# Optimization experiments

Hardware: AMD Instinct MI355X
Metric: run time of the kernel (lower is better)

Reference implementation:

```python
import jax, jax.numpy as jnp
import numpy as np

B, L, S, H, E, D = 2, 2048, 2048, 16, 64, 64


def setup_inputs() -> dict:
    key = jax.random.key(0)
    ks = jax.random.split(key, 6)
    return {
        "q1": jax.random.normal(ks[0], (B, L, H, E), dtype=jnp.float32),
        "k1": jax.random.normal(ks[1], (B, S, H, E), dtype=jnp.float32),
        "v1": jax.random.normal(ks[2], (B, S, H, D), dtype=jnp.float32),
        "q2": jax.random.normal(ks[3], (B, L, H, E), dtype=jnp.float32),
        "k2": jax.random.normal(ks[4], (B, S, H, E), dtype=jnp.float32),
        "v2": jax.random.normal(ks[5], (B, S, H, D), dtype=jnp.float32),
        "attn_mask": 0,  # accepted but unused by the original forward
    }


def reference(q1, k1, v1, q2, k2, v2, attn_mask):
    # scale = 1/sqrt(E) (self.scale is None in init_kwargs)
    scale = 1.0 / jnp.sqrt(jnp.asarray(q1.shape[-1], dtype=q1.dtype))
    # dual QK scores: [B,H,L,S]
    scores1 = jnp.einsum('blhe,bshe->bhls', q1, k1)
    scores2 = jnp.einsum('blhe,bshe->bhls', q2, k2)
    # eval-mode (dropout disabled for deterministic reference)
    A = jnp.tanh(scores1 * scale) * jax.nn.sigmoid(scores2 * scale)
    # weighted V matmul: [B,L,H,D]
    out = jnp.einsum('bhls,bshd->blhd', A, v1)
    return out
```

## Files before the change

kernel.cpp:

```cpp
#include <hip/hip_runtime.h>

constexpr int Bc = 2, Lc = 2048, Sc = 2048, Hc = 16, Ec = 64, Dc = 64;
constexpr int TILES = Sc / 64;
constexpr int NBH   = Bc * Hc;
constexpr size_t TILE_ELEMS = 4096;
constexpr size_t ARR_ELEMS  = (size_t)NBH * TILES * TILE_ELEMS;
constexpr size_t WS_NEED    = ARR_ELEMS * 2 * 3;

typedef float          f32x4  __attribute__((ext_vector_type(4)));
typedef __bf16         bf16x8 __attribute__((ext_vector_type(8)));
typedef unsigned short u16x8  __attribute__((ext_vector_type(8)));
typedef unsigned short u16x4  __attribute__((ext_vector_type(4)));
typedef unsigned int   u32x4  __attribute__((ext_vector_type(4)));
typedef unsigned int   u32x2  __attribute__((ext_vector_type(2)));

static __device__ __forceinline__ unsigned cvtpk(float lo, float hi) {
    unsigned r;
    asm("v_cvt_pk_bf16_f32 %0, %1, %2" : "=v"(r) : "v"(lo), "v"(hi));
    return r;
}

static __device__ __forceinline__ void gl2lds16(const void* g, void* l) {
    __builtin_amdgcn_global_load_lds(
        (const __attribute__((address_space(1))) unsigned int*)g,
        (__attribute__((address_space(3))) unsigned int*)l, 16, 0, 0);
}

static __device__ __forceinline__ float fexp2(float x) {
#if __has_builtin(__builtin_amdgcn_exp2f)
    return __builtin_amdgcn_exp2f(x);
#else
    return exp2f(x);
#endif
}

__global__ __launch_bounds__(256) void prepass_kernel(
    const float* __restrict__ k1, const float* __restrict__ k2,
    const float* __restrict__ v1,
    unsigned short* __restrict__ k1b, unsigned short* __restrict__ k2b,
    unsigned short* __restrict__ vb)
{
    __shared__ unsigned short vt[64 * 80];

    const int blk = blockIdx.x;
    const int st  = blk & 31;
    const int bh  = blk >> 5;
    const int b   = bh >> 4, h = bh & 15;
    const int s0  = st * 64;
    const size_t tileo = (size_t)blk * TILE_ELEMS;

    #pragma unroll
    for (int it = 0; it < 2; ++it) {
        int u  = threadIdx.x + it * 256;
        int s  = u >> 3, e8 = u & 7;
        size_t g = ((size_t)((b * Sc + s0 + s) * Hc + h)) * Ec + e8 * 8;

        float4 x0 = *reinterpret_cast<const float4*>(k1 + g);
        float4 x1 = *reinterpret_cast<const float4*>(k1 + g + 4);
        u32x4 o;
        o[0] = cvtpk(x0.x, x0.y); o[1] = cvtpk(x0.z, x0.w);
        o[2] = cvtpk(x1.x, x1.y); o[3] = cvtpk(x1.z, x1.w);
        *reinterpret_cast<u32x4*>(&k1b[tileo + (size_t)(s * 8 + (e8 ^ (s & 7))) * 8]) = o;

        x0 = *reinterpret_cast<const float4*>(k2 + g);
        x1 = *reinterpret_cast<const float4*>(k2 + g + 4);
        o[0] = cvtpk(x0.x, x0.y); o[1] = cvtpk(x0.z, x0.w);
        o[2] = cvtpk(x1.x, x1.y); o[3] = cvtpk(x1.z, x1.w);
        *reinterpret_cast<u32x4*>(&k2b[tileo + (size_t)(s * 8 + (e8 ^ (s & 7))) * 8]) = o;

        x0 = *reinterpret_cast<const float4*>(v1 + g);
        x1 = *reinterpret_cast<const float4*>(v1 + g + 4);
        o[0] = cvtpk(x0.x, x0.y); o[1] = cvtpk(x0.z, x0.w);
        o[2] = cvtpk(x1.x, x1.y); o[3] = cvtpk(x1.z, x1.w);
        *reinterpret_cast<u32x4*>(&vt[s * 80 + e8 * 8]) = o;
    }
    __syncthreads();

    #pragma unroll
    for (int it = 0; it < 2; ++it) {
        int u  = threadIdx.x + it * 256;
        int d  = u >> 3, sc8 = u & 7;
        u16x8 o;
        #pragma unroll
        for (int j = 0; j < 8; ++j) o[j] = vt[(sc8 * 8 + j) * 80 + d];
        *reinterpret_cast<u16x8*>(&vb[tileo + (size_t)(d * 8 + sc8) * 8]) = o;
    }
}

__global__ __launch_bounds__(256, 4) void fused_kernel(
    const float* __restrict__ q1, const float* __restrict__ q2,
    const unsigned short* __restrict__ k1b, const unsigned short* __restrict__ k2b,
    const unsigned short* __restrict__ vb, float* __restrict__ out)
{
    __shared__ unsigned short klds[2][2][4096];
    __shared__ unsigned int   pbounce[4][256];

    const int orig    = blockIdx.x;
    const int logical = (orig & 7) * 128 + (orig >> 3);
    const int lblk = logical & 31;
    const int bh   = logical >> 5;
    const int b    = bh >> 4, h = bh & 15;

    const int tid  = threadIdx.x;
    const int w    = tid >> 6;
    const int lane = tid & 63;
    const int lr   = lane & 15;
    const int lg   = lane >> 4;
    const int qsub = w >> 1;
    const int sh   = w & 1;

    constexpr float C1 = 0.36067376022224085f;
    constexpr float C2 = -0.18033688011112043f;
    bf16x8 a1[2][2], a2[2][2];
    #pragma unroll
    for (int qg = 0; qg < 2; ++qg) {
        const int    qrow  = lblk * 64 + qsub * 32 + qg * 16 + lr;
        const size_t qbase = ((size_t)((b * Lc + qrow) * Hc + h)) * Ec;
        #pragma unroll
        for (int es = 0; es < 2; ++es) {
            const float* p1 = q1 + qbase + es * 32 + lg * 8;
            const float* p2 = q2 + qbase + es * 32 + lg * 8;
            float4 x0 = *reinterpret_cast<const float4*>(p1);
            float4 x1 = *reinterpret_cast<const float4*>(p1 + 4);
            u32x4 o;
            o[0] = cvtpk(x0.x * C1, x0.y * C1); o[1] = cvtpk(x0.z * C1, x0.w * C1);
            o[2] = cvtpk(x1.x * C1, x1.y * C1); o[3] = cvtpk(x1.z * C1, x1.w * C1);
            a1[qg][es] = __builtin_bit_cast(bf16x8, o);
            x0 = *reinterpret_cast<const float4*>(p2);
            x1 = *reinterpret_cast<const float4*>(p2 + 4);
            o[0] = cvtpk(x0.x * C2, x0.y * C2); o[1] = cvtpk(x0.z * C2, x0.w * C2);
            o[2] = cvtpk(x1.x * C2, x1.y * C2); o[3] = cvtpk(x1.z * C2, x1.w * C2);
            a2[qg][es] = __builtin_bit_cast(bf16x8, o);
        }
    }

    f32x4 acc[2][4];
    #pragma unroll
    for (int qg = 0; qg < 2; ++qg)
        #pragma unroll
        for (int dt = 0; dt < 4; ++dt) acc[qg][dt] = (f32x4){0.f, 0.f, 0.f, 0.f};

    const unsigned short* k1g = k1b + (size_t)bh * TILES * TILE_ELEMS;
    const unsigned short* k2g = k2b + (size_t)bh * TILES * TILE_ELEMS;
    const unsigned short* vg  = vb  + (size_t)bh * TILES * TILE_ELEMS;
    unsigned int* pb = &pbounce[w][0];

    {
        const size_t tb = (size_t)tid * 8;
        gl2lds16(k1g + tb,        &klds[0][0][tid * 8]);
        gl2lds16(k1g + tb + 2048, &klds[0][0][tid * 8 + 2048]);
        gl2lds16(k2g + tb,        &klds[0][1][tid * 8]);
        gl2lds16(k2g + tb + 2048, &klds[0][1][tid * 8 + 2048]);
    }

    int cur = 0;
    for (int st = 0; st < TILES; ++st) {
        __syncthreads();
        if (st + 1 < TILES) {
            const size_t tb = (size_t)(st + 1) * TILE_ELEMS + tid * 8;
            const int nxt = cur ^ 1;
            gl2lds16(k1g + tb,        &klds[nxt][0][tid * 8]);
            gl2lds16(k1g + tb + 2048, &klds[nxt][0][tid * 8 + 2048]);
            gl2lds16(k2g + tb,        &klds[nxt][1][tid * 8]);
            gl2lds16(k2g + tb + 2048, &klds[nxt][1][tid * 8 + 2048]);
        }

        unsigned pq1[4];
        #pragma unroll
        for (int c = 0; c < 2; ++c) {
            f32x4 s1[2] = {{0.f,0.f,0.f,0.f},{0.f,0.f,0.f,0.f}};
            f32x4 s2[2] = {{0.f,0.f,0.f,0.f},{0.f,0.f,0.f,0.f}};
            #pragma unroll
            for (int es = 0; es < 2; ++es) {
                const int off = ((sh * 2 + c) * 16 + lr) * 64 + (((4 * es + lg) ^ (lr & 7)) * 8);
                bf16x8 kb1 = __builtin_bit_cast(bf16x8, *reinterpret_cast<const u16x8*>(&klds[cur][0][off]));
                bf16x8 kb2 = __builtin_bit_cast(bf16x8, *reinterpret_cast<const u16x8*>(&klds[cur][1][off]));
                #pragma unroll
                for (int qg = 0; qg < 2; ++qg) {
                    s1[qg] = __builtin_amdgcn_mfma_f32_16x16x32_bf16(kb1, a1[qg][es], s1[qg], 0, 0, 0);
                    s2[qg] = __builtin_amdgcn_mfma_f32_16x16x32_bf16(kb2, a2[qg][es], s2[qg], 0, 0, 0);
                }
            }
            #pragma unroll
            for (int qg = 0; qg < 2; ++qg) {
                float p[4];
                #pragma unroll
                for (int i = 0; i < 4; ++i) {
                    float t  = fexp2(s1[qg][i]);
                    float uu = fexp2(s2[qg][i]);
                    p[i] = (t - 1.f) * __builtin_amdgcn_rcpf((t + 1.f) * (1.f + uu));
                }
                unsigned w0 = cvtpk(p[0], p[1]);
                unsigned w1 = cvtpk(p[2], p[3]);
                if (qg == 0) {
                    *reinterpret_cast<u32x2*>(&pb[(c * 4 + lg) * 32 + 2 * lr]) = (u32x2){w0, w1};
                } else {
                    pq1[c * 2] = w0; pq1[c * 2 + 1] = w1;
                }
            }
        }

        u16x8 vfr[4];
        #pragma unroll
        for (int dt = 0; dt < 4; ++dt)
            vfr[dt] = *reinterpret_cast<const u16x8*>(
                &vg[(size_t)st * TILE_ELEMS + (dt * 16 + lr) * 64 + sh * 32 + lg * 8]);

        asm volatile("" ::: "memory");
        u32x2 r0 = *reinterpret_cast<const u32x2*>(&pb[(2 * lg) * 32 + 2 * lr]);
        u32x2 r1 = *reinterpret_cast<const u32x2*>(&pb[(2 * lg + 1) * 32 + 2 * lr]);
        bf16x8 pa0 = __builtin_bit_cast(bf16x8, (u32x4){r0[0], r0[1], r1[0], r1[1]});
        #pragma unroll
        for (int dt = 0; dt < 4; ++dt)
            acc[0][dt] = __builtin_amdgcn_mfma_f32_16x16x32_bf16(
                pa0, __builtin_bit_cast(bf16x8, vfr[dt]), acc[0][dt], 0, 0, 0);

        asm volatile("" ::: "memory");
        *reinterpret_cast<u32x2*>(&pb[(lg) * 32 + 2 * lr])     = (u32x2){pq1[0], pq1[1]};
        *reinterpret_cast<u32x2*>(&pb[(4 + lg) * 32 + 2 * lr]) = (u32x2){pq1[2], pq1[3]};
        asm volatile("" ::: "memory");
        r0 = *reinterpret_cast<const u32x2*>(&pb[(2 * lg) * 32 + 2 * lr]);
        r1 = *reinterpret_cast<const u32x2*>(&pb[(2 * lg + 1) * 32 + 2 * lr]);
        bf16x8 pa1 = __builtin_bit_cast(bf16x8, (u32x4){r0[0], r0[1], r1[0], r1[1]});
        #pragma unroll
        for (int dt = 0; dt < 4; ++dt)
            acc[1][dt] = __builtin_amdgcn_mfma_f32_16x16x32_bf16(
                pa1, __builtin_bit_cast(bf16x8, vfr[dt]), acc[1][dt], 0, 0, 0);

        cur ^= 1;
    }

    __syncthreads();
    float* mbuf = reinterpret_cast<float*>(&klds[0][0][0]);
    if (sh == 1) {
        #pragma unroll
        for (int qg = 0; qg < 2; ++qg)
            #pragma unroll
            for (int dt = 0; dt < 4; ++dt)
                *reinterpret_cast<f32x4*>(&mbuf[(((qsub * 2 + qg) * 4 + dt) * 256) + lane * 4]) = acc[qg][dt];
    }
    __syncthreads();
    if (sh == 0) {
        #pragma unroll
        for (int qg = 0; qg < 2; ++qg) {
            const int orow = lblk * 64 + qsub * 32 + qg * 16;
            #pragma unroll
            for (int dt = 0; dt < 4; ++dt) {
                f32x4 o = *reinterpret_cast<const f32x4*>(&mbuf[(((qsub * 2 + qg) * 4 + dt) * 256) + lane * 4]);
                o += acc[qg][dt];
                #pragma unroll
                for (int i = 0; i < 4; ++i) {
                    int l = orow + lg * 4 + i;
                    out[((size_t)(b * Lc + l) * Hc + h) * Dc + dt * 16 + lr] = o[i];
                }
            }
        }
    }
}

static __device__ __forceinline__ unsigned short f2bf(float f) {
    unsigned u = __builtin_bit_cast(unsigned, f);
    u += 0x7fffu + ((u >> 16) & 1u);
    return (unsigned short)(u >> 16);
}

__global__ __launch_bounds__(256) void fallback_kernel(
    const float* __restrict__ q1, const float* __restrict__ k1,
    const float* __restrict__ v1, const float* __restrict__ q2,
    const float* __restrict__ k2, float* __restrict__ out)
{
    constexpr int KSTR = 72, VSTR = 88, PSTR = 88;
    __shared__ unsigned short k1t[64 * KSTR];
    __shared__ unsigned short k2t[64 * KSTR];
    __shared__ unsigned short vtt[64 * VSTR];
    __shared__ unsigned short pt [4 * 16 * PSTR];

    const int blk  = blockIdx.x;
    const int lblk = blk & 31;
    const int bh   = blk >> 5;
    const int b    = bh >> 4;
    const int h    = bh & 15;
    const int tid  = threadIdx.x;
    const int w    = tid >> 6;
    const int lane = tid & 63;
    const int lr   = lane & 15;
    const int lg   = lane >> 4;

    const int    qrow  = lblk * 64 + w * 16 + lr;
    const size_t qbase = ((size_t)(b * Lc + qrow) * Hc + h) * Ec;
    bf16x8 a1[2], a2[2];
    for (int es = 0; es < 2; ++es) {
        u16x8 t1, t2;
        for (int j = 0; j < 8; ++j) {
            t1[j] = f2bf(q1[qbase + es * 32 + lg * 8 + j]);
            t2[j] = f2bf(q2[qbase + es * 32 + lg * 8 + j]);
        }
        a1[es] = __builtin_bit_cast(bf16x8, t1);
        a2[es] = __builtin_bit_cast(bf16x8, t2);
    }
    f32x4 acc[4];
    for (int i = 0; i < 4; ++i) acc[i] = (f32x4){0.f, 0.f, 0.f, 0.f};
    constexpr float CT = 0.25f, CS = -0.125f;

    for (int s0 = 0; s0 < Sc; s0 += 64) {
        for (int it = 0; it < 4; ++it) {
            int idx = tid + it * 256;
            int sr  = idx >> 4;
            int c4  = (idx & 15) << 2;
            size_t gk = ((size_t)(b * Sc + s0 + sr) * Hc + h) * Ec + c4;
            float4 x1 = *reinterpret_cast<const float4*>(k1 + gk);
            float4 x2 = *reinterpret_cast<const float4*>(k2 + gk);
            float4 xv = *reinterpret_cast<const float4*>(v1 + gk);
            u16x4 o1, o2;
            o1[0]=f2bf(x1.x); o1[1]=f2bf(x1.y); o1[2]=f2bf(x1.z); o1[3]=f2bf(x1.w);
            o2[0]=f2bf(x2.x); o2[1]=f2bf(x2.y); o2[2]=f2bf(x2.z); o2[3]=f2bf(x2.w);
            *reinterpret_cast<u16x4*>(&k1t[sr * KSTR + c4]) = o1;
            *reinterpret_cast<u16x4*>(&k2t[sr * KSTR + c4]) = o2;
            vtt[(c4 + 0) * VSTR + sr] = f2bf(xv.x);
            vtt[(c4 + 1) * VSTR + sr] = f2bf(xv.y);
            vtt[(c4 + 2) * VSTR + sr] = f2bf(xv.z);
            vtt[(c4 + 3) * VSTR + sr] = f2bf(xv.w);
        }
        __syncthreads();
        for (int ct = 0; ct < 4; ++ct) {
            f32x4 s1 = {0.f,0.f,0.f,0.f}, s2 = {0.f,0.f,0.f,0.f};
            for (int es = 0; es < 2; ++es) {
                bf16x8 b1 = __builtin_bit_cast(bf16x8,
                    *reinterpret_cast<const u16x8*>(&k1t[(ct*16 + lr) * KSTR + es*32 + lg*8]));
                bf16x8 b2 = __builtin_bit_cast(bf16x8,
                    *reinterpret_cast<const u16x8*>(&k2t[(ct*16 + lr) * KSTR + es*32 + lg*8]));
                s1 = __builtin_amdgcn_mfma_f32_16x16x32_bf16(a1[es], b1, s1, 0, 0, 0);
                s2 = __builtin_amdgcn_mfma_f32_16x16x32_bf16(a2[es], b2, s2, 0, 0, 0);
            }
            for (int i = 0; i < 4; ++i) {
                float xa = fminf(fmaxf(s1[i] * CT, -30.f), 30.f);
                float xb = fminf(fmaxf(s2[i] * CS, -30.f), 30.f);
                float t  = __expf(xa);
                float u  = __expf(xb);
                float p  = (t - 1.f) * __builtin_amdgcn_rcpf((t + 1.f) * (1.f + u));
                pt[(w*16 + lg*4 + i) * PSTR + ct*16 + lr] = f2bf(p);
            }
        }
        asm volatile("s_waitcnt lgkmcnt(0)" ::: "memory");
        for (int ks = 0; ks < 2; ++ks) {
            bf16x8 pa = __builtin_bit_cast(bf16x8,
                *reinterpret_cast<const u16x8*>(&pt[(w*16 + lr) * PSTR + ks*32 + lg*8]));
            for (int dt = 0; dt < 4; ++dt) {
                bf16x8 vf = __builtin_bit_cast(bf16x8,
                    *reinterpret_cast<const u16x8*>(&vtt[(dt*16 + lr) * VSTR + ks*32 + lg*8]));
                acc[dt] = __builtin_amdgcn_mfma_f32_16x16x32_bf16(pa, vf, acc[dt], 0, 0, 0);
            }
        }
        __syncthreads();
    }
    const int orow = lblk * 64 + w * 16;
    for (int dt = 0; dt < 4; ++dt)
        for (int i = 0; i < 4; ++i) {
            int l = orow + lg * 4 + i;
            out[((size_t)(b * Lc + l) * Hc + h) * Dc + dt * 16 + lr] = acc[dt][i];
        }
}

extern "C" void kernel_launch(void* const* d_in, const int* in_sizes, int n_in,
                              void* d_out, int out_size, void* d_ws, size_t ws_size,
                              hipStream_t stream) {
    const float* q1 = (const float*)d_in[0];
    const float* k1 = (const float*)d_in[1];
    const float* v1 = (const float*)d_in[2];
    const float* q2 = (const float*)d_in[3];
    const float* k2 = (const float*)d_in[4];
    float* out = (float*)d_out;

    if (ws_size >= WS_NEED) {
        unsigned short* k1b = (unsigned short*)d_ws;
        unsigned short* k2b = k1b + ARR_ELEMS;
        unsigned short* vbp = k2b + ARR_ELEMS;
        prepass_kernel<<<dim3(NBH * TILES), dim3(256), 0, stream>>>(k1, k2, v1, k1b, k2b, vbp);
        fused_kernel<<<dim3(NBH * TILES), dim3(256), 0, stream>>>(q1, q2, k1b, k2b, vbp, out);
    } else {
        fallback_kernel<<<dim3(NBH * TILES), dim3(256), 0, stream>>>(q1, k1, v1, q2, k2, out);
    }
}
```

Measured before the change: 115.3 us.

## Switch to 32x32x16 MFMA and pass P via permlane32 swap instead of LDS

Replaces the 16x16x32 bf16 MFMA tiling with 32x32x16 MFMAs for both the dual QK score products and the PV product. Each wave now covers a 32-query by 32-key block. The score-to-A-operand conversion uses v_permlane32_swap in registers instead of bouncing P through a per-wave LDS buffer, which removes LDS traffic and the pbounce shared array. The trade-off is larger accumulator register footprint and a changed output write pattern.

After: 122.8 us. 6.5% more time.

```diff
diff --git a/kernel.cpp b/kernel.cpp
--- a/kernel.cpp
+++ b/kernel.cpp
@@ -8,11 +8,11 @@
 constexpr size_t WS_NEED    = ARR_ELEMS * 2 * 3;
 
 typedef float          f32x4  __attribute__((ext_vector_type(4)));
+typedef float          f32x16 __attribute__((ext_vector_type(16)));
 typedef __bf16         bf16x8 __attribute__((ext_vector_type(8)));
 typedef unsigned short u16x8  __attribute__((ext_vector_type(8)));
 typedef unsigned short u16x4  __attribute__((ext_vector_type(4)));
 typedef unsigned int   u32x4  __attribute__((ext_vector_type(4)));
-typedef unsigned int   u32x2  __attribute__((ext_vector_type(2)));
 
 static __device__ __forceinline__ unsigned cvtpk(float lo, float hi) {
     unsigned r;
@@ -93,7 +93,6 @@
     const unsigned short* __restrict__ vb, float* __restrict__ out)
 {
     __shared__ unsigned short klds[2][2][4096];
-    __shared__ unsigned int   pbounce[4][256];
 
     const int orig    = blockIdx.x;
     const int logical = (orig & 7) * 128 + (orig >> 3);
@@ -104,46 +103,49 @@
     const int tid  = threadIdx.x;
     const int w    = tid >> 6;
     const int lane = tid & 63;
-    const int lr   = lane & 15;
-    const int lg   = lane >> 4;
+    const int l31  = lane & 31;
+    const int hi   = lane >> 5;
     const int qsub = w >> 1;
     const int sh   = w & 1;
 
     constexpr float C1 = 0.36067376022224085f;
     constexpr float C2 = -0.18033688011112043f;
-    bf16x8 a1[2][2], a2[2][2];
-    #pragma unroll
-    for (int qg = 0; qg < 2; ++qg) {
-        const int    qrow  = lblk * 64 + qsub * 32 + qg * 16 + lr;
-        const size_t qbase = ((size_t)((b * Lc + qrow) * Hc + h)) * Ec;
-        #pragma unroll
-        for (int es = 0; es < 2; ++es) {
-            const float* p1 = q1 + qbase + es * 32 + lg * 8;
-            const float* p2 = q2 + qbase + es * 32 + lg * 8;
-            float4 x0 = *reinterpret_cast<const float4*>(p1);
-            float4 x1 = *reinterpret_cast<const float4*>(p1 + 4);
-            u32x4 o;
-            o[0] = cvtpk(x0.x * C1, x0.y * C1); o[1] = cvtpk(x0.z * C1, x0.w * C1);
-            o[2] = cvtpk(x1.x * C1, x1.y * C1); o[3] = cvtpk(x1.z * C1, x1.w * C1);
-            a1[qg][es] = __builtin_bit_cast(bf16x8, o);
-            x0 = *reinterpret_cast<const float4*>(p2);
-            x1 = *reinterpret_cast<const float4*>(p2 + 4);
-            o[0] = cvtpk(x0.x * C2, x0.y * C2); o[1] = cvtpk(x0.z * C2, x0.w * C2);
-            o[2] = cvtpk(x1.x * C2, x1.y * C2); o[3] = cvtpk(x1.z * C2, x1.w * C2);
-            a2[qg][es] = __builtin_bit_cast(bf16x8, o);
-        }
-    }
-
-    f32x4 acc[2][4];
-    #pragma unroll
-    for (int qg = 0; qg < 2; ++qg)
-        #pragma unroll
-        for (int dt = 0; dt < 4; ++dt) acc[qg][dt] = (f32x4){0.f, 0.f, 0.f, 0.f};
+    const int    qrow  = lblk * 64 + qsub * 32 + l31;
+    const size_t qbase = ((size_t)((b * Lc + qrow) * Hc + h)) * Ec;
+    u32x4 qa1[4], qa2[4];
+    #pragma unroll
+    for (int es = 0; es < 4; ++es) {
+        const float* p1 = q1 + qbase + es * 16 + hi * 8;
+        const float* p2 = q2 + qbase + es * 16 + hi * 8;
+        float4 x0 = *reinterpret_cast<const float4*>(p1);
+        float4 x1 = *reinterpret_cast<const float4*>(p1 + 4);
+        qa1[es] = (u32x4){cvtpk(x0.x * C1, x0.y * C1), cvtpk(x0.z * C1, x0.w * C1),
+                          cvtpk(x1.x * C1, x1.y * C1), cvtpk(x1.z * C1, x1.w * C1)};
+        x0 = *reinterpret_cast<const float4*>(p2);
+        x1 = *reinterpret_cast<const float4*>(p2 + 4);
+        qa2[es] = (u32x4){cvtpk(x0.x * C2, x0.y * C2), cvtpk(x0.z * C2, x0.w * C2),
+                          cvtpk(x1.x * C2, x1.y * C2), cvtpk(x1.z * C2, x1.w * C2)};
+    }
+
+    f32x16 acc0 = {}, acc1 = {};
 
     const unsigned short* k1g = k1b + (size_t)bh * TILES * TILE_ELEMS;
     const unsigned short* k2g = k2b + (size_t)bh * TILES * TILE_ELEMS;
     const unsigned short* vg  = vb  + (size_t)bh * TILES * TILE_ELEMS;
-    unsigned int* pb = &pbounce[w][0];
+
+    const int srow = sh * 32 + l31;
+    const int swz  = srow & 7;
+    int koff[4];
+    #pragma unroll
+    for (int es = 0; es < 4; ++es)
+        koff[es] = (srow * 8 + ((es * 2 + hi) ^ swz)) * 8;
+
+    int voff[4];
+    #pragma unroll
+    for (int dt = 0; dt < 2; ++dt)
+        #pragma unroll
+        for (int ks = 0; ks < 2; ++ks)
+            voff[dt * 2 + ks] = (dt * 32 + l31) * 64 + sh * 32 + ks * 16 + hi * 8;
 
     {
         const size_t tb = (size_t)tid * 8;
@@ -165,67 +167,43 @@
             gl2lds16(k2g + tb + 2048, &klds[nxt][1][tid * 8 + 2048]);
         }
 
-        unsigned pq1[4];
-        #pragma unroll
-        for (int c = 0; c < 2; ++c) {
-            f32x4 s1[2] = {{0.f,0.f,0.f,0.f},{0.f,0.f,0.f,0.f}};
-            f32x4 s2[2] = {{0.f,0.f,0.f,0.f},{0.f,0.f,0.f,0.f}};
-            #pragma unroll
-            for (int es = 0; es < 2; ++es) {
-                const int off = ((sh * 2 + c) * 16 + lr) * 64 + (((4 * es + lg) ^ (lr & 7)) * 8);
-                bf16x8 kb1 = __builtin_bit_cast(bf16x8, *reinterpret_cast<const u16x8*>(&klds[cur][0][off]));
-                bf16x8 kb2 = __builtin_bit_cast(bf16x8, *reinterpret_cast<const u16x8*>(&klds[cur][1][off]));
-                #pragma unroll
-                for (int qg = 0; qg < 2; ++qg) {
-                    s1[qg] = __builtin_amdgcn_mfma_f32_16x16x32_bf16(kb1, a1[qg][es], s1[qg], 0, 0, 0);
-                    s2[qg] = __builtin_amdgcn_mfma_f32_16x16x32_bf16(kb2, a2[qg][es], s2[qg], 0, 0, 0);
-                }
-            }
-            #pragma unroll
-            for (int qg = 0; qg < 2; ++qg) {
-                float p[4];
-                #pragma unroll
-                for (int i = 0; i < 4; ++i) {
-                    float t  = fexp2(s1[qg][i]);
-                    float uu = fexp2(s2[qg][i]);
-                    p[i] = (t - 1.f) * __builtin_amdgcn_rcpf((t + 1.f) * (1.f + uu));
-                }
-                unsigned w0 = cvtpk(p[0], p[1]);
-                unsigned w1 = cvtpk(p[2], p[3]);
-                if (qg == 0) {
-                    *reinterpret_cast<u32x2*>(&pb[(c * 4 + lg) * 32 + 2 * lr]) = (u32x2){w0, w1};
-                } else {
-                    pq1[c * 2] = w0; pq1[c * 2 + 1] = w1;
-                }
-            }
-        }
-
+        const unsigned short* k1l = &klds[cur][0][0];
+        const unsigned short* k2l = &klds[cur][1][0];
+        f32x16 s1a = {}, s2a = {};
+        #pragma unroll
+        for (int es = 0; es < 4; ++es) {
+            bf16x8 kf1 = __builtin_bit_cast(bf16x8, *reinterpret_cast<const u16x8*>(&k1l[koff[es]]));
+            bf16x8 kf2 = __builtin_bit_cast(bf16x8, *reinterpret_cast<const u16x8*>(&k2l[koff[es]]));
+            s1a = __builtin_amdgcn_mfma_f32_32x32x16_bf16(kf1, __builtin_bit_cast(bf16x8, qa1[es]), s1a, 0, 0, 0);
+            s2a = __builtin_amdgcn_mfma_f32_32x32x16_bf16(kf2, __builtin_bit_cast(bf16x8, qa2[es]), s2a, 0, 0, 0);
+        }
+
+        const unsigned short* vt = vg + (size_t)st * TILE_ELEMS;
         u16x8 vfr[4];
         #pragma unroll
-        for (int dt = 0; dt < 4; ++dt)
-            vfr[dt] = *reinterpret_cast<const u16x8*>(
-                &vg[(size_t)st * TILE_ELEMS + (dt * 16 + lr) * 64 + sh * 32 + lg * 8]);
-
-        asm volatile("" ::: "memory");
-        u32x2 r0 = *reinterpret_cast<const u32x2*>(&pb[(2 * lg) * 32 + 2 * lr]);
-        u32x2 r1 = *reinterpret_cast<const u32x2*>(&pb[(2 * lg + 1) * 32 + 2 * lr]);
-        bf16x8 pa0 = __builtin_bit_cast(bf16x8, (u32x4){r0[0], r0[1], r1[0], r1[1]});
-        #pragma unroll
-        for (int dt = 0; dt < 4; ++dt)
-            acc[0][dt] = __builtin_amdgcn_mfma_f32_16x16x32_bf16(
-                pa0, __builtin_bit_cast(bf16x8, vfr[dt]), acc[0][dt], 0, 0, 0);
-
-        asm volatile("" ::: "memory");
-        *reinterpret_cast<u32x2*>(&pb[(lg) * 32 + 2 * lr])     = (u32x2){pq1[0], pq1[1]};
-        *reinterpret_cast<u32x2*>(&pb[(4 + lg) * 32 + 2 * lr]) = (u32x2){pq1[2], pq1[3]};
-        asm volatile("" ::: "memory");
-        r0 = *reinterpret_cast<const u32x2*>(&pb[(2 * lg) * 32 + 2 * lr]);
-        r1 = *reinterpret_cast<const u32x2*>(&pb[(2 * lg + 1) * 32 + 2 * lr]);
-        bf16x8 pa1 = __builtin_bit_cast(bf16x8, (u32x4){r0[0], r0[1], r1[0], r1[1]});
-        #pragma unroll
-        for (int dt = 0; dt < 4; ++dt)
-            acc[1][dt] = __builtin_amdgcn_mfma_f32_16x16x32_bf16(
-                pa1, __builtin_bit_cast(bf16x8, vfr[dt]), acc[1][dt], 0, 0, 0);
+        for (int i = 0; i < 4; ++i)
+            vfr[i] = *reinterpret_cast<const u16x8*>(&vt[voff[i]]);
+
+        float p[16];
+        #pragma unroll
+        for (int i = 0; i < 16; ++i) {
+            float t  = fexp2(s1a[i]);
+            float uu = fexp2(s2a[i]);
+            p[i] = (t - 1.f) * __builtin_amdgcn_rcpf((t + 1.f) * (1.f + uu));
+        }
+
+        #pragma unroll
+        for (int ks = 0; ks < 2; ++ks) {
+            unsigned A0 = cvtpk(p[8 * ks + 0], p[8 * ks + 1]);
+            unsigned A1 = cvtpk(p[8 * ks + 2], p[8 * ks + 3]);
+            unsigned B0 = cvtpk(p[8 * ks + 4], p[8 * ks + 5]);
+            unsigned B1 = cvtpk(p[8 * ks + 6], p[8 * ks + 7]);
+            asm("v_permlane32_swap_b32 %0, %1" : "+v"(A0), "+v"(B0));
+            asm("v_permlane32_swap_b32 %0, %1" : "+v"(A1), "+v"(B1));
+            bf16x8 pa = __builtin_bit_cast(bf16x8, (u32x4){A0, A1, B0, B1});
+            acc0 = __builtin_amdgcn_mfma_f32_32x32x16_bf16(pa, __builtin_bit_cast(bf16x8, vfr[ks]),     acc0, 0, 0, 0);
+            acc1 = __builtin_amdgcn_mfma_f32_32x32x16_bf16(pa, __builtin_bit_cast(bf16x8, vfr[2 + ks]), acc1, 0, 0, 0);
+        }
 
         cur ^= 1;
     }
@@ -234,25 +212,28 @@
     float* mbuf = reinterpret_cast<float*>(&klds[0][0][0]);
     if (sh == 1) {
         #pragma unroll
-        for (int qg = 0; qg < 2; ++qg)
-            #pragma unroll
-            for (int dt = 0; dt < 4; ++dt)
-                *reinterpret_cast<f32x4*>(&mbuf[(((qsub * 2 + qg) * 4 + dt) * 256) + lane * 4]) = acc[qg][dt];
+        for (int r4 = 0; r4 < 4; ++r4) {
+            *reinterpret_cast<f32x4*>(&mbuf[(qsub * 2 + 0) * 1024 + lane * 16 + r4 * 4]) =
+                (f32x4){acc0[r4 * 4 + 0], acc0[r4 * 4 + 1], acc0[r4 * 4 + 2], acc0[r4 * 4 + 3]};
+            *reinterpret_cast<f32x4*>(&mbuf[(qsub * 2 + 1) * 1024 + lane * 16 + r4 * 4]) =
+                (f32x4){acc1[r4 * 4 + 0], acc1[r4 * 4 + 1], acc1[r4 * 4 + 2], acc1[r4 * 4 + 3]};
+        }
     }
     __syncthreads();
     if (sh == 0) {
         #pragma unroll
-        for (int qg = 0; qg < 2; ++qg) {
-            const int orow = lblk * 64 + qsub * 32 + qg * 16;
+        for (int dt = 0; dt < 2; ++dt) {
+            float m[16];
             #pragma unroll
-            for (int dt = 0; dt < 4; ++dt) {
-                f32x4 o = *reinterpret_cast<const f32x4*>(&mbuf[(((qsub * 2 + qg) * 4 + dt) * 256) + lane * 4]);
-                o += acc[qg][dt];
-                #pragma unroll
-                for (int i = 0; i < 4; ++i) {
-                    int l = orow + lg * 4 + i;
-                    out[((size_t)(b * Lc + l) * Hc + h) * Dc + dt * 16 + lr] = o[i];
-                }
+            for (int r4 = 0; r4 < 4; ++r4) {
+                f32x4 v = *reinterpret_cast<const f32x4*>(&mbuf[(qsub * 2 + dt) * 1024 + lane * 16 + r4 * 4]);
+                m[r4 * 4 + 0] = v[0]; m[r4 * 4 + 1] = v[1]; m[r4 * 4 + 2] = v[2]; m[r4 * 4 + 3] = v[3];
+            }
+            #pragma unroll
+            for (int r = 0; r < 16; ++r) {
+                float val = m[r] + (dt == 0 ? acc0[r] : acc1[r]);
+                int q = lblk * 64 + qsub * 32 + (r & 3) + 8 * (r >> 2) + 4 * hi;
+                out[((size_t)(b * Lc + q) * Hc + h) * Dc + dt * 32 + l31] = val;
             }
         }
     }
```
